# Performance work log

Hardware: AMD Instinct MI355X
Metric: run time of the kernel (lower is better)

The kernel has to match this reference:

```python
import jax, jax.numpy as jnp
import numpy as np

HIDDEN = 2048
NUM_HEADS = 32
NUM_KV_HEADS = 8
GROUP = NUM_HEADS // NUM_KV_HEADS  # 4
HEAD_DIM = HIDDEN // NUM_HEADS     # 64
SEQ = 2048


def setup_inputs() -> dict:
    key = jax.random.key(0)
    ks = jax.random.split(key, 5)
    s = HIDDEN ** -0.5
    x = jax.random.normal(ks[0], (SEQ, HIDDEN), jnp.float32)
    q_proj = jax.random.normal(ks[1], (HIDDEN, HIDDEN), jnp.float32) * s
    k_proj = jax.random.normal(ks[2], (HIDDEN, HIDDEN // GROUP), jnp.float32) * s
    v_proj = jax.random.normal(ks[3], (HIDDEN, HIDDEN // GROUP), jnp.float32) * s
    o_proj = jax.random.normal(ks[4], (HIDDEN, HIDDEN), jnp.float32) * s
    # inv_freq = 1/rsqrt(10000**(i/d)) = sqrt(10000**(i/d)) per the original module
    inv_freq = jnp.sqrt(10000.0 ** (jnp.arange(0, HEAD_DIM, 2) / HEAD_DIM)).astype(jnp.float32)
    return {"x": x, "q_proj": q_proj, "k_proj": k_proj, "v_proj": v_proj,
            "o_proj": o_proj, "inv_freq": inv_freq}


def _rope(x, inv_freq):
    # x: [S, ..., HEAD_DIM]; rotation per the original (nonstandard) formula.
    orig_dtype = x.dtype
    x = x.astype(jnp.float32)
    seq = jnp.arange(x.shape[0])
    angles = seq[:, None] * jax.lax.stop_gradient(inv_freq)[None, :]  # [S, HEAD_DIM//2]
    bshape = (x.shape[0],) + (1,) * (x.ndim - 2) + (HEAD_DIM // 2,)
    sins = jnp.sin(angles).reshape(bshape)
    coss = jnp.cos(angles).reshape(bshape)
    half, odd = jnp.split(x, 2, axis=-1)
    out = jnp.concatenate([half * coss + odd * sins, half * sins - odd * coss], axis=-1)
    return out.astype(orig_dtype)


def reference(x, q_proj, k_proj, v_proj, o_proj, inv_freq):
    S = x.shape[0]
    q = (x @ q_proj).reshape(S, NUM_KV_HEADS, GROUP, HEAD_DIM)
    k = (x @ k_proj).reshape(S, NUM_KV_HEADS, HEAD_DIM)
    v = (x @ v_proj).reshape(S, NUM_KV_HEADS, HEAD_DIM)
    q = _rope(q, inv_freq)
    k = _rope(k, inv_freq)
    # scores: [a=S, b=S, h=kv_heads, g=group]
    scores = jnp.einsum('ahgd,bhd->abhg', q, k) / (HEAD_DIM ** 0.5)
    mask = jnp.tril(jnp.ones((S, S), dtype=jnp.bool_))[:, :, None, None]
    scores = jnp.where(mask, scores, -jnp.inf)
    attn = jax.nn.softmax(scores, axis=1)  # softmax over b (axis=-3)
    o = jnp.einsum('abhg,bhd->ahgd', attn, v).reshape(S, HIDDEN)
    return o @ o_proj
```

## Files before the change

kernel.cpp:

```cpp
#include <hip/hip_runtime.h>


typedef __bf16 bf16_t;
typedef __bf16 bf16x4 __attribute__((ext_vector_type(4)));
typedef __bf16 bf16x8 __attribute__((ext_vector_type(8)));
typedef float  f32x4  __attribute__((ext_vector_type(4)));
typedef short  s16x4  __attribute__((ext_vector_type(4)));

#define S_LEN   2048
#define HID     2048
#define NKV     8
#define NH      32
#define DHEAD   64
#define KVW     (NKV * DHEAD)

__device__ __align__(16) bf16_t g_xb [S_LEN * HID];
__device__ __align__(16) bf16_t g_wTq[HID * HID];
__device__ __align__(16) bf16_t g_wTk[KVW * HID];
__device__ __align__(16) bf16_t g_wTv[KVW * HID];
__device__ __align__(16) bf16_t g_wTo[HID * HID];
__device__ __align__(16) bf16_t g_q [S_LEN * HID];
__device__ __align__(16) bf16_t g_k [S_LEN * KVW];
__device__ __align__(16) bf16_t g_vT[KVW * S_LEN];
__device__ __align__(16) bf16_t g_om[S_LEN * HID];
__device__ float g_ropeC[S_LEN * 32];
__device__ float g_ropeS[S_LEN * 32];
__device__ __align__(16) float g_po[4u * S_LEN * HID];
__device__ float g_pl[4u * S_LEN * NH];

static __device__ inline s16x4 bc4(bf16x4 v) { s16x4 r; __builtin_memcpy(&r, &v, 8); return r; }

__device__ __forceinline__ void gll16(void* lds, const void* g) {
    __builtin_amdgcn_global_load_lds(
        (const __attribute__((address_space(1))) void*)g,
        (__attribute__((address_space(3))) void*)lds,
        16, 0, 0);
}

__global__ __launch_bounds__(256)
void prep_kernel(const float* __restrict__ x,
                 const float* __restrict__ qw, const float* __restrict__ kw,
                 const float* __restrict__ vw, const float* __restrict__ ow,
                 const void* __restrict__ invf_raw) {
    __shared__ bf16_t tile[64][65];
    int b = blockIdx.x, t = threadIdx.x;

    if (b < 256) {
        int idx = b * 256 + t;
        int s = idx >> 5, j = idx & 31;
        float f;
        if (*(const unsigned*)invf_raw == 0x3F800000u) {
            f = ((const float*)invf_raw)[j];
        } else {
            unsigned u = ((unsigned)((const unsigned short*)invf_raw)[j]) << 16;
            __builtin_memcpy(&f, &u, 4);
        }
        double a = (double)s * (double)f;
        g_ropeC[idx] = (float)cos(a);
        g_ropeS[idx] = (float)sin(a);
        return;
    }
    if (b < 4352) {
        int idx = (b - 256) * 256 + t;
        float4 v = reinterpret_cast<const float4*>(x)[idx];
        bf16x4 o;
        o[0] = (bf16_t)v.x; o[1] = (bf16_t)v.y; o[2] = (bf16_t)v.z; o[3] = (bf16_t)v.w;
        *reinterpret_cast<bf16x4*>(&g_xb[(size_t)idx * 4]) = o;
        return;
    }
    const float* in; bf16_t* outp; int R, C, tb;
    if (b < 5376)      { in = qw; outp = g_wTq; R = HID; C = HID; tb = b - 4352; }
    else if (b < 5632) { in = kw; outp = g_wTk; R = HID; C = KVW; tb = b - 5376; }
    else if (b < 5888) { in = vw; outp = g_wTv; R = HID; C = KVW; tb = b - 5632; }
    else               { in = ow; outp = g_wTo; R = HID; C = HID; tb = b - 5888; }
    int xt = C >> 6;
    int c0 = (tb % xt) * 64, r0 = (tb / xt) * 64;
    int tx = t & 63, ty = t >> 6;
    #pragma unroll
    for (int r = ty; r < 64; r += 4)
        tile[r][tx] = (bf16_t)in[(size_t)(r0 + r) * C + c0 + tx];
    __syncthreads();
    #pragma unroll
    for (int r = ty; r < 64; r += 4)
        outp[(size_t)(c0 + r) * R + r0 + tx] = tile[tx][r];
}

__global__ __launch_bounds__(256)
void gemm_fused_kernel(float* __restrict__ Cf, int which) {
    __shared__ __align__(16) bf16_t As[2][64 * 64];
    __shared__ __align__(16) bf16_t Bs[2][128 * 64];

    int t    = threadIdx.x;
    int lane = t & 63, wid = t >> 6;
    int quad = lane >> 4, l15 = lane & 15;
    int bx = blockIdx.x, m0 = blockIdx.y * 64;
    int wm = (wid >> 1) * 32, wn = (wid & 1) * 64;

    const bf16_t* A; const bf16_t* Bt; int n0;
    if (which == 1)      { A = g_om; Bt = g_wTo; n0 = bx * 128; }
    else {
        A = g_xb;
        if (bx < 16)      { Bt = g_wTq; n0 = bx * 128; }
        else if (bx < 20) { Bt = g_wTk; n0 = (bx - 16) * 128; }
        else              { Bt = g_wTv; n0 = (bx - 20) * 128; }
    }

    int crow = lane >> 3;
    int gseg = (lane & 7) ^ crow;
    int so   = l15 & 7;

    f32x4 acc[2][4];
    #pragma unroll
    for (int im = 0; im < 2; ++im)
        #pragma unroll
        for (int in = 0; in < 4; ++in)
            #pragma unroll
            for (int r = 0; r < 4; ++r) acc[im][in][r] = 0.f;

    auto stage = [&](int buf, int kt) {
        int ca0 = wid * 2, cb0 = wid * 4;
        gll16(&As[buf][(ca0 + 0) * 512], A  + (size_t)(m0 + (ca0 + 0) * 8 + crow) * HID + kt + gseg * 8);
        gll16(&As[buf][(ca0 + 1) * 512], A  + (size_t)(m0 + (ca0 + 1) * 8 + crow) * HID + kt + gseg * 8);
        gll16(&Bs[buf][(cb0 + 0) * 512], Bt + (size_t)(n0 + (cb0 + 0) * 8 + crow) * HID + kt + gseg * 8);
        gll16(&Bs[buf][(cb0 + 1) * 512], Bt + (size_t)(n0 + (cb0 + 1) * 8 + crow) * HID + kt + gseg * 8);
        gll16(&Bs[buf][(cb0 + 2) * 512], Bt + (size_t)(n0 + (cb0 + 2) * 8 + crow) * HID + kt + gseg * 8);
        gll16(&Bs[buf][(cb0 + 3) * 512], Bt + (size_t)(n0 + (cb0 + 3) * 8 + crow) * HID + kt + gseg * 8);
    };

    stage(0, 0);

    for (int it = 0; it < 32; ++it) {
        int cur = it & 1;
        __syncthreads();
        if (it + 1 < 32)
            stage(cur ^ 1, (it + 1) * 64);

        bf16x8 af[2][2], bfr[4][2];
        #pragma unroll
        for (int im = 0; im < 2; ++im)
            #pragma unroll
            for (int kh = 0; kh < 2; ++kh)
                af[im][kh] = *reinterpret_cast<const bf16x8*>(
                    &As[cur][(wm + im * 16 + l15) * 64 + (((kh * 4 + quad) ^ so) * 8)]);
        #pragma unroll
        for (int in = 0; in < 4; ++in)
            #pragma unroll
            for (int kh = 0; kh < 2; ++kh)
                bfr[in][kh] = *reinterpret_cast<const bf16x8*>(
                    &Bs[cur][(wn + in * 16 + l15) * 64 + (((kh * 4 + quad) ^ so) * 8)]);
        #pragma unroll
        for (int im = 0; im < 2; ++im)
            #pragma unroll
            for (int in = 0; in < 4; ++in)
                #pragma unroll
                for (int kh = 0; kh < 2; ++kh)
                    acc[im][in] = __builtin_amdgcn_mfma_f32_16x16x32_bf16(
                        af[im][kh], bfr[in][kh], acc[im][in], 0, 0, 0);
    }

    if (which == 1) {
        #pragma unroll
        for (int im = 0; im < 2; ++im) {
            int rowb = m0 + wm + im * 16 + quad * 4;
            #pragma unroll
            for (int in = 0; in < 4; ++in) {
                int col = bx * 128 + wn + in * 16 + l15;
                #pragma unroll
                for (int r = 0; r < 4; ++r)
                    Cf[(size_t)(rowb + r) * HID + col] = acc[im][in][r];
            }
        }
    } else if (bx < 20) {
        bf16_t* Cb; int N, colbase;
        if (bx < 16) { Cb = g_q; N = HID; colbase = bx * 128 + wn; }
        else         { Cb = g_k; N = KVW; colbase = (bx - 16) * 128 + wn; }
        #pragma unroll
        for (int im = 0; im < 2; ++im) {
            #pragma unroll
            for (int r = 0; r < 4; ++r) {
                int row = m0 + wm + im * 16 + quad * 4 + r;
                #pragma unroll
                for (int in = 0; in < 2; ++in) {
                    int d = in * 16 + l15;
                    float a  = acc[im][in][r];
                    float bb = acc[im][in + 2][r];
                    float cc = g_ropeC[row * 32 + d];
                    float ss = g_ropeS[row * 32 + d];
                    Cb[(size_t)row * N + colbase + d]      = (bf16_t)(a * cc + bb * ss);
                    Cb[(size_t)row * N + colbase + 32 + d] = (bf16_t)(a * ss - bb * cc);
                }
            }
        }
    } else {
        #pragma unroll
        for (int im = 0; im < 2; ++im) {
            int rowb = m0 + wm + im * 16 + quad * 4;
            #pragma unroll
            for (int in = 0; in < 4; ++in) {
                int col = (bx - 20) * 128 + wn + in * 16 + l15;
                #pragma unroll
                for (int r = 0; r < 4; ++r)
                    g_vT[(size_t)col * S_LEN + (rowb + r)] = (bf16_t)acc[im][in][r];
            }
        }
    }
}

__global__ __launch_bounds__(256)
void flash_part_kernel() {
    __shared__ __align__(16) bf16_t Ks[64][72];
    __shared__ __align__(16) bf16_t Vs[64][72];

    int t    = threadIdx.x;
    int lane = t & 63, wid = t >> 6;
    int quad = lane >> 4, l15 = lane & 15;
    int bx   = blockIdx.x;
    int hk   = bx & 7;
    int qb32 = (bx >> 3) & 63;
    int chunk = bx >> 9;
    int nkt  = (qb32 >> 1) + 1;
    int kt0  = chunk * 8;
    if (kt0 >= nkt) return;
    int kt1  = min(kt0 + 8, nkt);

    int head = hk * 4 + wid;
    int q0   = qb32 * 32;

    bf16x8 aq[2][2];
    #pragma unroll
    for (int mq = 0; mq < 2; ++mq) {
        const bf16_t* qp = g_q + (size_t)(q0 + mq * 16 + l15) * HID + head * 64 + quad * 8;
        aq[mq][0] = *reinterpret_cast<const bf16x8*>(qp);
        aq[mq][1] = *reinterpret_cast<const bf16x8*>(qp + 32);
        #pragma unroll
        for (int j = 0; j < 8; ++j) {
            aq[mq][0][j] = (bf16_t)((float)aq[mq][0][j] * 0.125f);
            aq[mq][1][j] = (bf16_t)((float)aq[mq][1][j] * 0.125f);
        }
    }

    bf16x4 ones4;
    #pragma unroll
    for (int j = 0; j < 4; ++j) ones4[j] = (bf16_t)1.0f;
    s16x4 ones_s = bc4(ones4);

    f32x4 oacc[2][4], liacc[2];
    #pragma unroll
    for (int mq = 0; mq < 2; ++mq) {
        #pragma unroll
        for (int r = 0; r < 4; ++r) liacc[mq][r] = 0.f;
        #pragma unroll
        for (int dt = 0; dt < 4; ++dt)
            #pragma unroll
            for (int r = 0; r < 4; ++r) oacc[mq][dt][r] = 0.f;
    }

    int qcol[2] = { q0 + l15, q0 + 16 + l15 };

    for (int kt = kt0; kt < kt1; ++kt) {
        int k0 = kt * 64;
        __syncthreads();
        #pragma unroll
        for (int i = t; i < 512; i += 256) {
            int row = i >> 3, seg = i & 7;
            *reinterpret_cast<int4*>(&Ks[row][seg * 8]) =
                *reinterpret_cast<const int4*>(g_k + (size_t)(k0 + row) * KVW + hk * 64 + seg * 8);
            *reinterpret_cast<int4*>(&Vs[row][seg * 8]) =
                *reinterpret_cast<const int4*>(g_vT + (size_t)(hk * 64 + row) * S_LEN + k0 + seg * 8);
        }
        __syncthreads();

        bf16x8 ak[4][2];
        #pragma unroll
        for (int mk = 0; mk < 4; ++mk) {
            ak[mk][0] = *reinterpret_cast<const bf16x8*>(&Ks[mk * 16 + l15][quad * 8]);
            ak[mk][1] = *reinterpret_cast<const bf16x8*>(&Ks[mk * 16 + l15][32 + quad * 8]);
        }

        f32x4 sacc[4][2];
        #pragma unroll
        for (int mk = 0; mk < 4; ++mk)
            #pragma unroll
            for (int mq = 0; mq < 2; ++mq) {
                f32x4 s;
                #pragma unroll
                for (int r = 0; r < 4; ++r) s[r] = 0.f;
                s = __builtin_amdgcn_mfma_f32_16x16x32_bf16(ak[mk][0], aq[mq][0], s, 0, 0, 0);
                s = __builtin_amdgcn_mfma_f32_16x16x32_bf16(ak[mk][1], aq[mq][1], s, 0, 0, 0);
                sacc[mk][mq] = s;
            }

        s16x4 pas[4][2];
        #pragma unroll
        for (int mk = 0; mk < 4; ++mk)
            #pragma unroll
            for (int mq = 0; mq < 2; ++mq) {
                bf16x4 pa;
                #pragma unroll
                for (int r = 0; r < 4; ++r) {
                    int kk = k0 + mk * 16 + quad * 4 + r;
                    pa[r] = (bf16_t)((kk <= qcol[mq]) ? __expf(sacc[mk][mq][r] - 16.0f) : 0.0f);
                }
                pas[mk][mq] = bc4(pa);
            }

        #pragma unroll
        for (int mk = 0; mk < 4; ++mk) {
            #pragma unroll
            for (int dt = 0; dt < 4; ++dt) {
                bf16x4 bv = *reinterpret_cast<const bf16x4*>(&Vs[dt * 16 + l15][mk * 16 + quad * 4]);
                s16x4 bvs = bc4(bv);
                #pragma unroll
                for (int mq = 0; mq < 2; ++mq)
                    oacc[mq][dt] = __builtin_amdgcn_mfma_f32_16x16x16bf16_1k(pas[mk][mq], bvs, oacc[mq][dt], 0, 0, 0);
            }
            #pragma unroll
            for (int mq = 0; mq < 2; ++mq)
                liacc[mq] = __builtin_amdgcn_mfma_f32_16x16x16bf16_1k(pas[mk][mq], ones_s, liacc[mq], 0, 0, 0);
        }
    }

    float* po = g_po + (size_t)chunk * S_LEN * HID;
    #pragma unroll
    for (int mq = 0; mq < 2; ++mq)
        #pragma unroll
        for (int r = 0; r < 4; ++r) {
            int row = q0 + mq * 16 + quad * 4 + r;
            #pragma unroll
            for (int dt = 0; dt < 4; ++dt)
                po[(size_t)row * HID + head * 64 + dt * 16 + l15] = oacc[mq][dt][r];
            if (l15 == 0)
                g_pl[((size_t)chunk * S_LEN + row) * NH + head] = liacc[mq][r];
        }
}

__global__ __launch_bounds__(256)
void flash_combine_kernel() {
    int t = blockIdx.x * 256 + threadIdx.x;
    int row  = t >> 9;
    int col4 = (t & 511) * 4;
    int head = col4 >> 6;
    int nkt  = ((row >> 5) >> 1) + 1;
    int nc   = (nkt + 7) >> 3;

    float4 s = make_float4(0.f, 0.f, 0.f, 0.f);
    float l = 0.f;
    for (int c = 0; c < nc; ++c) {
        const float4 v = *reinterpret_cast<const float4*>(
            g_po + ((size_t)c * S_LEN + row) * HID + col4);
        s.x += v.x; s.y += v.y; s.z += v.z; s.w += v.w;
        l += g_pl[((size_t)c * S_LEN + row) * NH + head];
    }
    float inv = 1.0f / l;
    bf16x4 o;
    o[0] = (bf16_t)(s.x * inv); o[1] = (bf16_t)(s.y * inv);
    o[2] = (bf16_t)(s.z * inv); o[3] = (bf16_t)(s.w * inv);
    *reinterpret_cast<bf16x4*>(&g_om[(size_t)row * HID + col4]) = o;
}

extern "C" void kernel_launch(void* const* d_in, const int* in_sizes, int n_in,
                              void* d_out, int out_size, void* d_ws, size_t ws_size,
                              hipStream_t stream) {
    const float* x    = (const float*)d_in[0];
    const float* qpW  = (const float*)d_in[1];
    const float* kpW  = (const float*)d_in[2];
    const float* vpW  = (const float*)d_in[3];
    const float* opW  = (const float*)d_in[4];
    const void*  invf = d_in[5];
    float* out = (float*)d_out;

    prep_kernel<<<6912, 256, 0, stream>>>(x, qpW, kpW, vpW, opW, invf);
    gemm_fused_kernel<<<dim3(24, 32), 256, 0, stream>>>(nullptr, 0);
    flash_part_kernel<<<2048, 256, 0, stream>>>();
    flash_combine_kernel<<<4096, 256, 0, stream>>>();
    gemm_fused_kernel<<<dim3(16, 32), 256, 0, stream>>>(out, 1);
}
```

Baseline: 253.8 us.

## Enlarge GEMM block tile to 128x128 and use explicit vmcnt waits

Doubles the M dimension of each GEMM block so every wave computes a 64x64 output tile, halving the grid for both the QKV and output projections and increasing operand reuse from LDS. The single __syncthreads is replaced by an s_waitcnt vmcnt(8) that waits only for the current buffer's loads, plus two s_barriers. This reduces global and LDS traffic per FLOP, at the cost of more accumulator registers, more LDS, and fewer blocks than CUs for the output GEMM, which can cause load imbalance.

```diff
diff --git a/kernel.cpp b/kernel.cpp
--- a/kernel.cpp
+++ b/kernel.cpp
@@ -87,14 +87,14 @@
 
 __global__ __launch_bounds__(256)
 void gemm_fused_kernel(float* __restrict__ Cf, int which) {
-    __shared__ __align__(16) bf16_t As[2][64 * 64];
+    __shared__ __align__(16) bf16_t As[2][128 * 64];
     __shared__ __align__(16) bf16_t Bs[2][128 * 64];
 
     int t    = threadIdx.x;
     int lane = t & 63, wid = t >> 6;
     int quad = lane >> 4, l15 = lane & 15;
-    int bx = blockIdx.x, m0 = blockIdx.y * 64;
-    int wm = (wid >> 1) * 32, wn = (wid & 1) * 64;
+    int bx = blockIdx.x, m0 = blockIdx.y * 128;
+    int wm = (wid >> 1) * 64, wn = (wid & 1) * 64;
 
     const bf16_t* A; const bf16_t* Bt; int n0;
     if (which == 1)      { A = g_om; Bt = g_wTo; n0 = bx * 128; }
@@ -109,58 +109,61 @@
     int gseg = (lane & 7) ^ crow;
     int so   = l15 & 7;
 
-    f32x4 acc[2][4];
-    #pragma unroll
-    for (int im = 0; im < 2; ++im)
+    f32x4 acc[4][4];
+    #pragma unroll
+    for (int im = 0; im < 4; ++im)
         #pragma unroll
         for (int in = 0; in < 4; ++in)
             #pragma unroll
             for (int r = 0; r < 4; ++r) acc[im][in][r] = 0.f;
 
     auto stage = [&](int buf, int kt) {
-        int ca0 = wid * 2, cb0 = wid * 4;
-        gll16(&As[buf][(ca0 + 0) * 512], A  + (size_t)(m0 + (ca0 + 0) * 8 + crow) * HID + kt + gseg * 8);
-        gll16(&As[buf][(ca0 + 1) * 512], A  + (size_t)(m0 + (ca0 + 1) * 8 + crow) * HID + kt + gseg * 8);
-        gll16(&Bs[buf][(cb0 + 0) * 512], Bt + (size_t)(n0 + (cb0 + 0) * 8 + crow) * HID + kt + gseg * 8);
-        gll16(&Bs[buf][(cb0 + 1) * 512], Bt + (size_t)(n0 + (cb0 + 1) * 8 + crow) * HID + kt + gseg * 8);
-        gll16(&Bs[buf][(cb0 + 2) * 512], Bt + (size_t)(n0 + (cb0 + 2) * 8 + crow) * HID + kt + gseg * 8);
-        gll16(&Bs[buf][(cb0 + 3) * 512], Bt + (size_t)(n0 + (cb0 + 3) * 8 + crow) * HID + kt + gseg * 8);
+        int c0 = wid * 4;
+        #pragma unroll
+        for (int c = 0; c < 4; ++c) {
+            gll16(&As[buf][(c0 + c) * 512],
+                  A  + (size_t)(m0 + (c0 + c) * 8 + crow) * HID + kt + gseg * 8);
+            gll16(&Bs[buf][(c0 + c) * 512],
+                  Bt + (size_t)(n0 + (c0 + c) * 8 + crow) * HID + kt + gseg * 8);
+        }
     };
 
     stage(0, 0);
 
     for (int it = 0; it < 32; ++it) {
         int cur = it & 1;
-        __syncthreads();
-        if (it + 1 < 32)
+        if (it + 1 < 32) {
             stage(cur ^ 1, (it + 1) * 64);
-
-        bf16x8 af[2][2], bfr[4][2];
-        #pragma unroll
-        for (int im = 0; im < 2; ++im)
-            #pragma unroll
-            for (int kh = 0; kh < 2; ++kh)
-                af[im][kh] = *reinterpret_cast<const bf16x8*>(
-                    &As[cur][(wm + im * 16 + l15) * 64 + (((kh * 4 + quad) ^ so) * 8)]);
-        #pragma unroll
-        for (int in = 0; in < 4; ++in)
-            #pragma unroll
-            for (int kh = 0; kh < 2; ++kh)
-                bfr[in][kh] = *reinterpret_cast<const bf16x8*>(
-                    &Bs[cur][(wn + in * 16 + l15) * 64 + (((kh * 4 + quad) ^ so) * 8)]);
-        #pragma unroll
-        for (int im = 0; im < 2; ++im)
-            #pragma unroll
-            for (int in = 0; in < 4; ++in)
-                #pragma unroll
-                for (int kh = 0; kh < 2; ++kh)
+            asm volatile("s_waitcnt vmcnt(8)" ::: "memory");
+        } else {
+            asm volatile("s_waitcnt vmcnt(0)" ::: "memory");
+        }
+        asm volatile("s_barrier" ::: "memory");
+
+        #pragma unroll
+        for (int kh = 0; kh < 2; ++kh) {
+            bf16x8 af[4], bfv[4];
+            #pragma unroll
+            for (int i = 0; i < 4; ++i) {
+                af[i]  = *reinterpret_cast<const bf16x8*>(
+                    &As[cur][(wm + i * 16 + l15) * 64 + (((kh * 4 + quad) ^ so) * 8)]);
+                bfv[i] = *reinterpret_cast<const bf16x8*>(
+                    &Bs[cur][(wn + i * 16 + l15) * 64 + (((kh * 4 + quad) ^ so) * 8)]);
+            }
+            #pragma unroll
+            for (int im = 0; im < 4; ++im)
+                #pragma unroll
+                for (int in = 0; in < 4; ++in)
                     acc[im][in] = __builtin_amdgcn_mfma_f32_16x16x32_bf16(
-                        af[im][kh], bfr[in][kh], acc[im][in], 0, 0, 0);
+                        af[im], bfv[in], acc[im][in], 0, 0, 0);
+        }
+
+        asm volatile("s_barrier" ::: "memory");
     }
 
     if (which == 1) {
         #pragma unroll
-        for (int im = 0; im < 2; ++im) {
+        for (int im = 0; im < 4; ++im) {
             int rowb = m0 + wm + im * 16 + quad * 4;
             #pragma unroll
             for (int in = 0; in < 4; ++in) {
@@ -175,7 +178,7 @@
         if (bx < 16) { Cb = g_q; N = HID; colbase = bx * 128 + wn; }
         else         { Cb = g_k; N = KVW; colbase = (bx - 16) * 128 + wn; }
         #pragma unroll
-        for (int im = 0; im < 2; ++im) {
+        for (int im = 0; im < 4; ++im) {
             #pragma unroll
             for (int r = 0; r < 4; ++r) {
                 int row = m0 + wm + im * 16 + quad * 4 + r;
@@ -193,7 +196,7 @@
         }
     } else {
         #pragma unroll
-        for (int im = 0; im < 2; ++im) {
+        for (int im = 0; im < 4; ++im) {
             int rowb = m0 + wm + im * 16 + quad * 4;
             #pragma unroll
             for (int in = 0; in < 4; ++in) {
@@ -370,8 +373,8 @@
     float* out = (float*)d_out;
 
     prep_kernel<<<6912, 256, 0, stream>>>(x, qpW, kpW, vpW, opW, invf);
-    gemm_fused_kernel<<<dim3(24, 32), 256, 0, stream>>>(nullptr, 0);
+    gemm_fused_kernel<<<dim3(24, 16), 256, 0, stream>>>(nullptr, 0);
     flash_part_kernel<<<2048, 256, 0, stream>>>();
     flash_combine_kernel<<<4096, 256, 0, stream>>>();
-    gemm_fused_kernel<<<dim3(16, 32), 256, 0, stream>>>(out, 1);
-}
+    gemm_fused_kernel<<<dim3(16, 16), 256, 0, stream>>>(out, 1);
+}
```

New measurement: 257.0 us. Within noise of the previous version (+1.2%).
